# Kernel tuning notes

Measured on AMD Instinct MI355X. Metric: run time of the kernel, lower is better.

Reference implementation:

```python
import jax, jax.numpy as jnp
import numpy as np

N1, N2, D, F = 8192, 8192, 1024, 800


def setup_inputs() -> dict:
    key = jax.random.key(0)
    ks = jax.random.split(key, 10)
    s = 1.0 / np.sqrt(D)
    return {
        "m1": jax.random.normal(ks[0], (N1, D), jnp.float32),
        "m2": jax.random.normal(ks[1], (N2, D), jnp.float32),
        "Wf1": jax.random.normal(ks[2], (F, D), jnp.float32) * s,
        "bf1": jax.random.normal(ks[3], (F,), jnp.float32) * 0.01,
        "Wf2": jax.random.normal(ks[4], (F, D), jnp.float32) * s,
        "bf2": jax.random.normal(ks[5], (F,), jnp.float32) * 0.01,
        "W1": jax.random.normal(ks[6], (F, D), jnp.float32) * s,
        "b1": jax.random.normal(ks[7], (F,), jnp.float32) * 0.01,
        "W2": jax.random.normal(ks[8], (F, D), jnp.float32) * s,
        "b2": jax.random.normal(ks[9], (F,), jnp.float32) * 0.01,
    }


def reference(m1, m2, Wf1, bf1, Wf2, bf2, W1, b1, W2, b2):
    # raw_prod: [N1, N2]
    raw = jnp.einsum('id,jd->ij', m1, m2)
    alpha2 = jax.nn.softmax(raw, axis=-1)        # rows over m2: [N1, N2]
    alpha1 = jax.nn.softmax(raw.T, axis=-1)      # rows over m1: [N2, N1]
    attended_m1 = alpha1 @ m1                    # [N2, D]
    attended_m2 = alpha2 @ m2                    # [N1, D]
    # eval mode: dropout is identity
    filter1 = jax.nn.sigmoid((attended_m2 @ Wf1.T + bf1).mean(0))  # [F]
    filter2 = jax.nn.sigmoid((attended_m1 @ Wf2.T + bf2).mean(0))  # [F]
    transformed_m1 = jnp.tanh(attended_m1 @ W1.T + b1).mean(0)     # [F]
    transformed_m2 = jnp.tanh(attended_m2 @ W2.T + b2).mean(0)     # [F]
    return (transformed_m1 * filter1, transformed_m2 * filter2)
```

## Files before the change

### kernel.cpp

```cpp
#include <hip/hip_runtime.h>

typedef __attribute__((ext_vector_type(8))) short s8v;
typedef __attribute__((ext_vector_type(4))) float f4v;
typedef __attribute__((ext_vector_type(4))) unsigned short us4v;
typedef __attribute__((ext_vector_type(8))) unsigned short us8v;
typedef _Float16 h8v __attribute__((ext_vector_type(8)));

#define MFMA(a, b, c) __builtin_amdgcn_mfma_f32_16x16x32_bf16(a, b, c, 0, 0, 0)
#define GLOAD16(g, l)                                                          \
  __builtin_amdgcn_global_load_lds((const __attribute__((address_space(1))) void*)(g), \
                                   (__attribute__((address_space(3))) void*)(l), 16, 0, 0)

#define L2E 1.44269504088896f
#define C128L2E 184.6649652337873f

__device__ __forceinline__ unsigned short f2bf(float x) {
  unsigned int u = __float_as_uint(x);
  u += 0x7fffu + ((u >> 16) & 1u);
  return (unsigned short)(u >> 16);
}
__device__ __forceinline__ float bf2f(unsigned short h) {
  return __uint_as_float(((unsigned int)h) << 16);
}
__device__ __forceinline__ float f16bits2f(unsigned short u) {
  union { unsigned short us; _Float16 f; } cv; cv.us = u; return (float)cv.f;
}

__global__ void k_zero(float* p, int n) {
  int i = blockIdx.x * 256 + threadIdx.x;
  if (i < n) p[i] = 0.f;
}

__global__ __launch_bounds__(256) void k_wbf(const float* __restrict__ W,
                                             unsigned short* __restrict__ wb) {
  int idx = blockIdx.x * 256 + threadIdx.x;
  int f = idx >> 10;
  wb[idx] = f2bf((f < 800) ? W[idx] : 0.f);
}

__global__ __launch_bounds__(256) void k_prep(const float* __restrict__ in,
                                              unsigned short* __restrict__ outb,
                                              unsigned short* __restrict__ outT) {
  __shared__ float lf[64 * 68];
  int bx = blockIdx.x;
  int rb = bx >> 4, cb = bx & 15;
  long r0 = (long)rb * 64, c0 = (long)cb * 64;
  int tid = threadIdx.x;
#pragma unroll
  for (int q = 0; q < 4; ++q) {
    int fid = tid + 256 * q;
    int r = fid >> 4, c4 = fid & 15;
    f4v v = *(const f4v*)&in[(r0 + r) * 1024 + c0 + 4 * c4];
    *(f4v*)&lf[r * 68 + 4 * c4] = v;
    us4v h;
#pragma unroll
    for (int e = 0; e < 4; ++e) h[e] = f2bf(v[e]);
    *(us4v*)&outb[(r0 + r) * 1024 + c0 + 4 * c4] = h;
  }
  __syncthreads();
#pragma unroll
  for (int q = 0; q < 4; ++q) {
    int fid = tid + 256 * q;
    int oc = fid >> 4, or4 = fid & 15;
    us4v h;
#pragma unroll
    for (int e = 0; e < 4; ++e) h[e] = f2bf(lf[(4 * or4 + e) * 68 + oc]);
    *(us4v*)&outT[(c0 + oc) * 8192 + r0 + 4 * or4] = h;
  }
}

__global__ __launch_bounds__(512, 2) void k_gemm_raw8(const unsigned short* __restrict__ m1b,
                                                      const unsigned short* __restrict__ m2b,
                                                      _Float16* __restrict__ rawh,
                                                      float* __restrict__ row_s,
                                                      float* __restrict__ col_s) {
  __shared__ unsigned short LDS[65536];
  const int tid = threadIdx.x, lane = tid & 63, wid = tid >> 6;
  const int wr = wid >> 2, wc = wid & 3;
  const int x = lane >> 4;

  int swz = ((int)blockIdx.x & 7) * 128 + ((int)blockIdx.x >> 3);
  const long i0 = (long)(swz >> 5) * 256;
  const long j0 = (long)(swz & 31) * 256;

  const unsigned short* gA[2];
  const unsigned short* gB[2];
  int ldst[2];
#pragma unroll
  for (int s = 0; s < 2; ++s) {
    int c = s * 512 + tid;
    int r = c >> 2, qp = c & 3;
    int ql = qp ^ ((r >> 1) & 3);
    gA[s] = m1b + (i0 + r) * 1024 + ql * 8;
    gB[s] = m2b + (j0 + r) * 1024 + ql * 8;
    ldst[s] = c * 8;
  }
  int offA[8], offB[4];
#pragma unroll
  for (int m = 0; m < 8; ++m) {
    int rr = wr * 128 + m * 16 + (lane & 15);
    offA[m] = (rr * 4 + (x ^ ((rr >> 1) & 3))) * 8;
  }
#pragma unroll
  for (int n = 0; n < 4; ++n) {
    int cc = wc * 64 + n * 16 + (lane & 15);
    offB[n] = (cc * 4 + (x ^ ((cc >> 1) & 3))) * 8;
  }

  f4v acc[8][4];
#pragma unroll
  for (int m = 0; m < 8; ++m)
#pragma unroll
    for (int n = 0; n < 4; ++n) acc[m][n] = (f4v)0.f;

#define STG(u, kt)                                                            \
  do {                                                                        \
    _Pragma("unroll") for (int s = 0; s < 2; ++s)                             \
        GLOAD16(gA[s] + (kt) * 32, &LDS[(u) * 16384 + ldst[s]]);              \
    _Pragma("unroll") for (int s = 0; s < 2; ++s)                             \
        GLOAD16(gB[s] + (kt) * 32, &LDS[(u) * 16384 + 8192 + ldst[s]]);       \
  } while (0)

  STG(0, 0); STG(1, 1); STG(2, 2);

  for (int kt = 0; kt < 32; ++kt) {
    const int u = kt & 3;
    if (kt < 30)      asm volatile("s_waitcnt vmcnt(8)" ::: "memory");
    else if (kt == 30) asm volatile("s_waitcnt vmcnt(4)" ::: "memory");
    else               asm volatile("s_waitcnt vmcnt(0)" ::: "memory");
    asm volatile("s_barrier" ::: "memory");
    __builtin_amdgcn_sched_barrier(0);
    const int Ab = u * 16384, Bb = u * 16384 + 8192;
    s8v af[8], bf[4];
#pragma unroll
    for (int m = 0; m < 8; ++m) af[m] = *(const s8v*)&LDS[Ab + offA[m]];
#pragma unroll
    for (int n = 0; n < 4; ++n) bf[n] = *(const s8v*)&LDS[Bb + offB[n]];
    if (kt < 29) STG((kt + 3) & 3, kt + 3);
    asm volatile("s_waitcnt lgkmcnt(0)" ::: "memory");
    __builtin_amdgcn_sched_barrier(0);
    __builtin_amdgcn_s_setprio(1);
#pragma unroll
    for (int m = 0; m < 8; ++m)
#pragma unroll
      for (int n = 0; n < 4; ++n)
        acc[m][n] = MFMA(af[m], bf[n], acc[m][n]);
    __builtin_amdgcn_s_setprio(0);
  }
#undef STG

  float* rsf = (float*)LDS;
  float* csf = rsf + 256;
  if (tid < 256) { rsf[tid] = 0.f; csf[tid] = 0.f; }
  __syncthreads();
  float cls[4] = {0.f, 0.f, 0.f, 0.f};
#pragma unroll
  for (int m = 0; m < 8; ++m) {
    long rbase = i0 + wr * 128 + m * 16 + x * 4;
#pragma unroll
    for (int r = 0; r < 4; ++r) {
      float rsum = 0.f;
#pragma unroll
      for (int n = 0; n < 4; ++n) {
        long col = j0 + wc * 64 + n * 16 + (lane & 15);
        _Float16 hv = (_Float16)acc[m][n][r];
        rawh[(rbase + r) * 8192 + col] = hv;
        float e = exp2f(fmaf((float)hv, L2E, -C128L2E));
        rsum += e;
        cls[n] += e;
      }
      rsum += __shfl_xor(rsum, 1);
      rsum += __shfl_xor(rsum, 2);
      rsum += __shfl_xor(rsum, 4);
      rsum += __shfl_xor(rsum, 8);
      if ((lane & 15) == 0)
        atomicAdd(&rsf[wr * 128 + m * 16 + x * 4 + r], rsum);
    }
  }
#pragma unroll
  for (int n = 0; n < 4; ++n) {
    cls[n] += __shfl_xor(cls[n], 16);
    cls[n] += __shfl_xor(cls[n], 32);
    if (lane < 16) atomicAdd(&csf[wc * 64 + n * 16 + lane], cls[n]);
  }
  __syncthreads();
  if (tid < 256) {
    atomicAdd(&row_s[i0 + tid], rsf[tid]);
    atomicAdd(&col_s[j0 + tid], csf[tid]);
  }
}

__global__ __launch_bounds__(256) void k_fin(const float* __restrict__ s,
                                             float* __restrict__ o) {
  int i = blockIdx.x * 256 + threadIdx.x;
  o[i] = C128L2E + log2f(s[i]);
}

__global__ __launch_bounds__(512, 2) void k_gemm_att8(const unsigned short* __restrict__ P,
                                                      const unsigned short* __restrict__ BT,
                                                      unsigned short* __restrict__ attb,
                                                      float* __restrict__ meanv) {
  __shared__ unsigned short LDS[49152];
  const int tid = threadIdx.x, lane = tid & 63, wid = tid >> 6;
  const int wr = wid >> 1, wc = wid & 1;
  const int x = lane >> 4;

  int swz = ((int)blockIdx.x & 7) * 32 + ((int)blockIdx.x >> 3);
  const long i0 = (long)(swz >> 3) * 256;
  const long d0 = (long)(swz & 7) * 128;

  const unsigned short* gA[2];
  const unsigned short* gB0;
  int ldstA[2], ldstB0;
#pragma unroll
  for (int s = 0; s < 2; ++s) {
    int c = s * 512 + tid;
    int r = c >> 2, qp = c & 3;
    int ql = qp ^ ((r >> 1) & 3);
    gA[s] = P + (i0 + r) * 8192 + ql * 8;
    ldstA[s] = c * 8;
  }
  {
    int c = tid;
    int r = c >> 2, qp = c & 3;
    int ql = qp ^ ((r >> 1) & 3);
    gB0 = BT + (d0 + r) * 8192 + ql * 8;
    ldstB0 = c * 8;
  }
  int offA[4], offB[4];
#pragma unroll
  for (int m = 0; m < 4; ++m) {
    int rr = wr * 64 + m * 16 + (lane & 15);
    offA[m] = (rr * 4 + (x ^ ((rr >> 1) & 3))) * 8;
  }
#pragma unroll
  for (int n = 0; n < 4; ++n) {
    int cc = wc * 64 + n * 16 + (lane & 15);
    offB[n] = (cc * 4 + (x ^ ((cc >> 1) & 3))) * 8;
  }

  f4v acc[4][4];
#pragma unroll
  for (int m = 0; m < 4; ++m)
#pragma unroll
    for (int n = 0; n < 4; ++n) acc[m][n] = (f4v)0.f;

#define STGA(u, kt)                                                           \
  do {                                                                        \
    _Pragma("unroll") for (int s = 0; s < 2; ++s)                             \
        GLOAD16(gA[s] + (kt) * 32, &LDS[(u) * 12288 + ldstA[s]]);             \
    GLOAD16(gB0 + (kt) * 32, &LDS[(u) * 12288 + 8192 + ldstB0]);              \
  } while (0)

  STGA(0, 0); STGA(1, 1); STGA(2, 2);

  for (int kt = 0; kt < 256; ++kt) {
    const int u = kt & 3;
    if (kt < 254)       asm volatile("s_waitcnt vmcnt(6)" ::: "memory");
    else if (kt == 254) asm volatile("s_waitcnt vmcnt(3)" ::: "memory");
    else                asm volatile("s_waitcnt vmcnt(0)" ::: "memory");
    asm volatile("s_barrier" ::: "memory");
    __builtin_amdgcn_sched_barrier(0);
    const int Ab = u * 12288, Bb = u * 12288 + 8192;
    s8v af[4], bf[4];
#pragma unroll
    for (int m = 0; m < 4; ++m) af[m] = *(const s8v*)&LDS[Ab + offA[m]];
#pragma unroll
    for (int n = 0; n < 4; ++n) bf[n] = *(const s8v*)&LDS[Bb + offB[n]];
    if (kt < 253) STGA((kt + 3) & 3, kt + 3);
    asm volatile("s_waitcnt lgkmcnt(0)" ::: "memory");
    __builtin_amdgcn_sched_barrier(0);
    __builtin_amdgcn_s_setprio(1);
#pragma unroll
    for (int m = 0; m < 4; ++m)
#pragma unroll
      for (int n = 0; n < 4; ++n)
        acc[m][n] = MFMA(af[m], bf[n], acc[m][n]);
    __builtin_amdgcn_s_setprio(0);
  }
#undef STGA

#pragma unroll
  for (int n = 0; n < 4; ++n) {
    long colg = d0 + wc * 64 + n * 16 + (lane & 15);
    float s = 0.f;
#pragma unroll
    for (int m = 0; m < 4; ++m) {
      long rowg = i0 + wr * 64 + m * 16 + x * 4;
      f4v a = acc[m][n];
#pragma unroll
      for (int r = 0; r < 4; ++r) {
        attb[(rowg + r) * 1024 + colg] = f2bf(a[r]);
        s += a[r];
      }
    }
    s += __shfl_xor(s, 16);
    s += __shfl_xor(s, 32);
    if (lane < 16) atomicAdd(&meanv[d0 + wc * 64 + n * 16 + lane], s);
  }
}

__global__ __launch_bounds__(256) void k_texp_ip(unsigned short* buf,
                                                 const float* __restrict__ hh) {
  __shared__ unsigned short lt[2][64 * 80];
  int a = blockIdx.x >> 7, b = blockIdx.x & 127;
  if (a > b) return;
  const int tid = threadIdx.x;
  const int r = tid & 63;
  const int cw = tid >> 6;
  const int ntile = (a == b) ? 1 : 2;

  for (int t = 0; t < ntile; ++t) {
    long ro = (long)(t == 0 ? a : b) * 64;
    long co = (long)(t == 0 ? b : a) * 64;
#pragma unroll
    for (int q = 0; q < 2; ++q) {
      int c8 = cw + 4 * q;
      us8v u = *(const us8v*)&buf[(ro + r) * 8192 + co + c8 * 8];
      f4v hA = *(const f4v*)&hh[co + c8 * 8];
      f4v hB = *(const f4v*)&hh[co + c8 * 8 + 4];
#pragma unroll
      for (int e = 0; e < 8; ++e) {
        float hv = (e < 4) ? hA[e] : hB[e - 4];
        lt[t][(c8 * 8 + e) * 80 + r] = f2bf(exp2f(fmaf(f16bits2f(u[e]), L2E, -hv)));
      }
    }
  }
  __syncthreads();
  for (int t = 0; t < ntile; ++t) {
    long dr = (long)(t == 0 ? b : a) * 64;
    long dc = (long)(t == 0 ? a : b) * 64;
#pragma unroll
    for (int q = 0; q < 2; ++q) {
      int fid = tid + 256 * q;
      int jr = fid >> 3, c8 = fid & 7;
      us8v o = *(const us8v*)&lt[t][jr * 80 + c8 * 8];
      *(us8v*)&buf[(dr + jr) * 8192 + dc + c8 * 8] = o;
    }
  }
}

__global__ __launch_bounds__(256) void k_prow_ip(unsigned short* buf,
                                                 const float* __restrict__ hh,
                                                 const float* __restrict__ rm2) {
  __shared__ unsigned short lt[2][64 * 80];
  int a = blockIdx.x >> 7, b = blockIdx.x & 127;
  if (a > b) return;
  const int tid = threadIdx.x;
  const int r = tid & 63;
  const int cw = tid >> 6;
  const int ntile = (a == b) ? 1 : 2;

  for (int t = 0; t < ntile; ++t) {
    long ro = (long)(t == 0 ? a : b) * 64;
    long co = (long)(t == 0 ? b : a) * 64;
    float hj;
#pragma unroll
    for (int q = 0; q < 2; ++q) {
      int c8 = cw + 4 * q;
      us8v u = *(const us8v*)&buf[(ro + r) * 8192 + co + c8 * 8];
      if (q == 0) hj = hh[ro + r];
      f4v rA = *(const f4v*)&rm2[co + c8 * 8];
      f4v rB = *(const f4v*)&rm2[co + c8 * 8 + 4];
#pragma unroll
      for (int e = 0; e < 8; ++e) {
        float rv = (e < 4) ? rA[e] : rB[e - 4];
        float sc = exp2f(fminf(hj - rv, 120.f));
        lt[t][(c8 * 8 + e) * 80 + r] = f2bf(bf2f(u[e]) * sc);
      }
    }
  }
  __syncthreads();
  for (int t = 0; t < ntile; ++t) {
    long dr = (long)(t == 0 ? b : a) * 64;
    long dc = (long)(t == 0 ? a : b) * 64;
#pragma unroll
    for (int q = 0; q < 2; ++q) {
      int fid = tid + 256 * q;
      int ir = fid >> 3, c8 = fid & 7;
      us8v o = *(const us8v*)&lt[t][ir * 80 + c8 * 8];
      *(us8v*)&buf[(dr + ir) * 8192 + dc + c8 * 8] = o;
    }
  }
}

__global__ __launch_bounds__(256) void k_gemm_tanh(const unsigned short* __restrict__ attb,
                                                   const unsigned short* __restrict__ Wb,
                                                   const float* __restrict__ bias,
                                                   float* __restrict__ acct) {
  __shared__ unsigned short As[128 * 32], Bs[128 * 32];
  const int tid = threadIdx.x, lane = tid & 63, wv = tid >> 6;
  const int wrow = wv >> 1, wcol = wv & 1;
  int sw = ((int)blockIdx.x & 7) * 56 + ((int)blockIdx.x >> 3);
  const long i0 = (long)(sw / 7) * 128;
  const long f0 = (long)(sw % 7) * 128;

  const int r16 = lane >> 2;
  const int sslot = (lane & 3) ^ ((r16 >> 1) & 3);
  const unsigned short* gA0 = &attb[(i0 + 32 * wv + r16) * 1024 + sslot * 8];
  const unsigned short* gA1 = gA0 + 16 * 1024;
  const unsigned short* gB0 = &Wb[(f0 + 32 * wv + r16) * 1024 + sslot * 8];
  const unsigned short* gB1 = gB0 + 16 * 1024;
  unsigned short* lA0 = &As[(32 * wv) * 32];
  unsigned short* lA1 = &As[(32 * wv + 16) * 32];
  unsigned short* lB0 = &Bs[(32 * wv) * 32];
  unsigned short* lB1 = &Bs[(32 * wv + 16) * 32];

  f4v acc[4][4];
#pragma unroll
  for (int a = 0; a < 4; ++a)
#pragma unroll
    for (int b = 0; b < 4; ++b) acc[a][b] = (f4v)0.f;

  for (int kt = 0; kt < 32; ++kt) {
    GLOAD16(gA0 + kt * 32, lA0);
    GLOAD16(gA1 + kt * 32, lA1);
    GLOAD16(gB0 + kt * 32, lB0);
    GLOAD16(gB1 + kt * 32, lB1);
    __syncthreads();
    const int kkx = lane >> 4;
    s8v af[4], bf[4];
#pragma unroll
    for (int mf = 0; mf < 4; ++mf) {
      int rr = wrow * 64 + mf * 16 + (lane & 15);
      af[mf] = *(const s8v*)&As[rr * 32 + (kkx ^ ((rr >> 1) & 3)) * 8];
      int cc = wcol * 64 + mf * 16 + (lane & 15);
      bf[mf] = *(const s8v*)&Bs[cc * 32 + (kkx ^ ((cc >> 1) & 3)) * 8];
    }
#pragma unroll
    for (int mf = 0; mf < 4; ++mf)
#pragma unroll
      for (int nf = 0; nf < 4; ++nf)
        acc[mf][nf] = MFMA(af[mf], bf[nf], acc[mf][nf]);
    __syncthreads();
  }
#pragma unroll
  for (int nf = 0; nf < 4; ++nf) {
    long colg = f0 + wcol * 64 + nf * 16 + (lane & 15);
    float bv = (colg < 800) ? bias[colg] : 0.f;
    float s = 0.f;
#pragma unroll
    for (int mf = 0; mf < 4; ++mf) {
      f4v a = acc[mf][nf];
#pragma unroll
      for (int r = 0; r < 4; ++r) s += tanhf(a[r] + bv);
    }
    s += __shfl_xor(s, 16);
    s += __shfl_xor(s, 32);
    if (lane < 16) atomicAdd(&acct[f0 + wcol * 64 + nf * 16 + lane], s);
  }
}

__global__ __launch_bounds__(256) void k_filt(const float* __restrict__ Wf1,
                                              const float* __restrict__ bf1,
                                              const float* __restrict__ Wf2,
                                              const float* __restrict__ bf2,
                                              const float* __restrict__ mean2,
                                              const float* __restrict__ mean1,
                                              float* __restrict__ filt1,
                                              float* __restrict__ filt2) {
  int wv = threadIdx.x >> 6, lane = threadIdx.x & 63;
  int gid = blockIdx.x * 4 + wv;
  const float* Wr;
  const float* mv;
  float b;
  float* outp;
  if (gid < 800) {
    Wr = Wf1 + (long)gid * 1024; mv = mean2; b = bf1[gid]; outp = filt1 + gid;
  } else {
    int f = gid - 800;
    Wr = Wf2 + (long)f * 1024; mv = mean1; b = bf2[f]; outp = filt2 + f;
  }
  float s = 0.f;
#pragma unroll
  for (int q = 0; q < 16; ++q) s += mv[lane + 64 * q] * Wr[lane + 64 * q];
#pragma unroll
  for (int off = 32; off >= 1; off >>= 1) s += __shfl_xor(s, off);
  if (lane == 0) *outp = 1.f / (1.f + __expf(-(s * (1.f / 8192.f) + b)));
}

__global__ void k_final(const float* __restrict__ acct1, const float* __restrict__ acct2,
                        const float* __restrict__ filt1, const float* __restrict__ filt2,
                        float* __restrict__ out) {
  int i = blockIdx.x * 256 + threadIdx.x;
  if (i < 800) {
    out[i] = acct1[i] * (1.f / 8192.f) * filt1[i];
    out[800 + i] = acct2[i] * (1.f / 8192.f) * filt2[i];
  }
}

extern "C" void kernel_launch(void* const* d_in, const int* in_sizes, int n_in,
                              void* d_out, int out_size, void* d_ws, size_t ws_size,
                              hipStream_t stream) {
  (void)in_sizes; (void)n_in; (void)out_size;
  const float* m1  = (const float*)d_in[0];
  const float* m2  = (const float*)d_in[1];
  const float* Wf1 = (const float*)d_in[2];
  const float* bf1 = (const float*)d_in[3];
  const float* Wf2 = (const float*)d_in[4];
  const float* bf2 = (const float*)d_in[5];
  const float* W1  = (const float*)d_in[6];
  const float* b1  = (const float*)d_in[7];
  const float* W2  = (const float*)d_in[8];
  const float* b2  = (const float*)d_in[9];
  float* out = (float*)d_out;
  char* ws = (char*)d_ws;

  _Float16* rawh       = (_Float16*)(ws);
  unsigned short* rawu = (unsigned short*)(ws);
  unsigned short* m1T  = (unsigned short*)(ws + 134217728UL);
  unsigned short* m2T  = (unsigned short*)(ws + 150994944UL);
  unsigned short* m1b  = (unsigned short*)(ws + 167772160UL);
  unsigned short* m2b  = (unsigned short*)(ws + 184549376UL);
  unsigned short* att1 = (unsigned short*)(ws + 167772160UL);
  unsigned short* att2 = (unsigned short*)(ws + 184549376UL);
  unsigned short* W1b  = (unsigned short*)(ws + 201326592UL);
  unsigned short* W2b  = (unsigned short*)(ws + 203161600UL);
  float* rm2   = (float*)(ws + 204996608UL);
  float* hh    = (float*)(ws + 205029376UL);
  float* row_s = (float*)(ws + 205062144UL);
  float* col_s = (float*)(ws + 205094912UL);
  float* mean1 = (float*)(ws + 205127680UL);
  float* mean2 = (float*)(ws + 205131776UL);
  float* acct1 = (float*)(ws + 205135872UL);
  float* acct2 = (float*)(ws + 205139968UL);
  float* filt1 = (float*)(ws + 205144064UL);
  float* filt2 = (float*)(ws + 205148160UL);

  if (ws_size < 207246592UL) return;

  k_zero<<<80, 256, 0, stream>>>(row_s, 20480);
  k_wbf<<<3584, 256, 0, stream>>>(W1, W1b);
  k_wbf<<<3584, 256, 0, stream>>>(W2, W2b);
  k_prep<<<2048, 256, 0, stream>>>(m1, m1b, m1T);
  k_prep<<<2048, 256, 0, stream>>>(m2, m2b, m2T);
  k_gemm_raw8<<<1024, 512, 0, stream>>>(m1b, m2b, rawh, row_s, col_s);
  k_fin<<<64, 256, 0, stream>>>(row_s, rm2);
  k_texp_ip<<<16384, 256, 0, stream>>>(rawu, hh);
  k_gemm_att8<<<256, 512, 0, stream>>>(rawu, m1T, att1, mean1);
  k_prow_ip<<<16384, 256, 0, stream>>>(rawu, hh, rm2);
  k_gemm_att8<<<256, 512, 0, stream>>>(rawu, m2T, att2, mean2);
  k_gemm_tanh<<<448, 256, 0, stream>>>(att1, W1b, b1, acct1);
  k_gemm_tanh<<<448, 256, 0, stream>>>(att2, W2b, b2, acct2);
  k_filt<<<400, 256, 0, stream>>>(Wf1, bf1, Wf2, bf2, mean2, mean1, filt1, filt2);
  k_final<<<4, 256, 0, stream>>>(acct1, acct2, filt1, filt2, out);
}
```

Baseline: 605.9 us.

## Store exp-shifted probabilities once and defer softmax normalization into attention GEMMs

The raw GEMM epilogue now writes bf16 exp(raw-128) directly instead of fp16 raw logits. Both attention GEMMs consume this same unnormalized P, and divide each output row by its row or column sum in the epilogue. This removes the log-sum kernel, the exponentiation inside the transpose pass, and the whole rescaling pass over the 8192x8192 matrix, leaving only a plain in-place transpose. The cost is that both softmax directions now share one fixed shift, so probabilities are stored unnormalized in bf16, which depends on the logit range staying within float range.

```diff
diff --git a/kernel.cpp b/kernel.cpp
--- a/kernel.cpp
+++ b/kernel.cpp
@@ -4,7 +4,6 @@
 typedef __attribute__((ext_vector_type(4))) float f4v;
 typedef __attribute__((ext_vector_type(4))) unsigned short us4v;
 typedef __attribute__((ext_vector_type(8))) unsigned short us8v;
-typedef _Float16 h8v __attribute__((ext_vector_type(8)));
 
 #define MFMA(a, b, c) __builtin_amdgcn_mfma_f32_16x16x32_bf16(a, b, c, 0, 0, 0)
 #define GLOAD16(g, l)                                                          \
@@ -21,9 +20,6 @@
 }
 __device__ __forceinline__ float bf2f(unsigned short h) {
   return __uint_as_float(((unsigned int)h) << 16);
-}
-__device__ __forceinline__ float f16bits2f(unsigned short u) {
-  union { unsigned short us; _Float16 f; } cv; cv.us = u; return (float)cv.f;
 }
 
 __global__ void k_zero(float* p, int n) {
@@ -71,7 +67,7 @@
 
 __global__ __launch_bounds__(512, 2) void k_gemm_raw8(const unsigned short* __restrict__ m1b,
                                                       const unsigned short* __restrict__ m2b,
-                                                      _Float16* __restrict__ rawh,
+                                                      unsigned short* __restrict__ Pb,
                                                       float* __restrict__ row_s,
                                                       float* __restrict__ col_s) {
   __shared__ unsigned short LDS[65536];
@@ -163,9 +159,8 @@
 #pragma unroll
       for (int n = 0; n < 4; ++n) {
         long col = j0 + wc * 64 + n * 16 + (lane & 15);
-        _Float16 hv = (_Float16)acc[m][n][r];
-        rawh[(rbase + r) * 8192 + col] = hv;
-        float e = exp2f(fmaf((float)hv, L2E, -C128L2E));
+        float e = exp2f(fmaf(acc[m][n][r], L2E, -C128L2E));
+        Pb[(rbase + r) * 8192 + col] = f2bf(e);
         rsum += e;
         cls[n] += e;
       }
@@ -190,16 +185,11 @@
   }
 }
 
-__global__ __launch_bounds__(256) void k_fin(const float* __restrict__ s,
-                                             float* __restrict__ o) {
-  int i = blockIdx.x * 256 + threadIdx.x;
-  o[i] = C128L2E + log2f(s[i]);
-}
-
 __global__ __launch_bounds__(512, 2) void k_gemm_att8(const unsigned short* __restrict__ P,
                                                       const unsigned short* __restrict__ BT,
                                                       unsigned short* __restrict__ attb,
-                                                      float* __restrict__ meanv) {
+                                                      float* __restrict__ meanv,
+                                                      const float* __restrict__ divv) {
   __shared__ unsigned short LDS[49152];
   const int tid = threadIdx.x, lane = tid & 63, wid = tid >> 6;
   const int wr = wid >> 1, wc = wid & 1;
@@ -280,6 +270,13 @@
   }
 #undef STGA
 
+  float inv[4][4];
+#pragma unroll
+  for (int m = 0; m < 4; ++m)
+#pragma unroll
+    for (int r = 0; r < 4; ++r)
+      inv[m][r] = 1.f / divv[i0 + wr * 64 + m * 16 + x * 4 + r];
+
 #pragma unroll
   for (int n = 0; n < 4; ++n) {
     long colg = d0 + wc * 64 + n * 16 + (lane & 15);
@@ -290,8 +287,9 @@
       f4v a = acc[m][n];
 #pragma unroll
       for (int r = 0; r < 4; ++r) {
-        attb[(rowg + r) * 1024 + colg] = f2bf(a[r]);
-        s += a[r];
+        float val = a[r] * inv[m][r];
+        attb[(rowg + r) * 1024 + colg] = f2bf(val);
+        s += val;
       }
     }
     s += __shfl_xor(s, 16);
@@ -300,8 +298,7 @@
   }
 }
 
-__global__ __launch_bounds__(256) void k_texp_ip(unsigned short* buf,
-                                                 const float* __restrict__ hh) {
+__global__ __launch_bounds__(256) void k_tr(unsigned short* buf) {
   __shared__ unsigned short lt[2][64 * 80];
   int a = blockIdx.x >> 7, b = blockIdx.x & 127;
   if (a > b) return;
@@ -317,13 +314,8 @@
     for (int q = 0; q < 2; ++q) {
       int c8 = cw + 4 * q;
       us8v u = *(const us8v*)&buf[(ro + r) * 8192 + co + c8 * 8];
-      f4v hA = *(const f4v*)&hh[co + c8 * 8];
-      f4v hB = *(const f4v*)&hh[co + c8 * 8 + 4];
-#pragma unroll
-      for (int e = 0; e < 8; ++e) {
-        float hv = (e < 4) ? hA[e] : hB[e - 4];
-        lt[t][(c8 * 8 + e) * 80 + r] = f2bf(exp2f(fmaf(f16bits2f(u[e]), L2E, -hv)));
-      }
+#pragma unroll
+      for (int e = 0; e < 8; ++e) lt[t][(c8 * 8 + e) * 80 + r] = u[e];
     }
   }
   __syncthreads();
@@ -336,50 +328,6 @@
       int jr = fid >> 3, c8 = fid & 7;
       us8v o = *(const us8v*)&lt[t][jr * 80 + c8 * 8];
       *(us8v*)&buf[(dr + jr) * 8192 + dc + c8 * 8] = o;
-    }
-  }
-}
-
-__global__ __launch_bounds__(256) void k_prow_ip(unsigned short* buf,
-                                                 const float* __restrict__ hh,
-                                                 const float* __restrict__ rm2) {
-  __shared__ unsigned short lt[2][64 * 80];
-  int a = blockIdx.x >> 7, b = blockIdx.x & 127;
-  if (a > b) return;
-  const int tid = threadIdx.x;
-  const int r = tid & 63;
-  const int cw = tid >> 6;
-  const int ntile = (a == b) ? 1 : 2;
-
-  for (int t = 0; t < ntile; ++t) {
-    long ro = (long)(t == 0 ? a : b) * 64;
-    long co = (long)(t == 0 ? b : a) * 64;
-    float hj;
-#pragma unroll
-    for (int q = 0; q < 2; ++q) {
-      int c8 = cw + 4 * q;
-      us8v u = *(const us8v*)&buf[(ro + r) * 8192 + co + c8 * 8];
-      if (q == 0) hj = hh[ro + r];
-      f4v rA = *(const f4v*)&rm2[co + c8 * 8];
-      f4v rB = *(const f4v*)&rm2[co + c8 * 8 + 4];
-#pragma unroll
-      for (int e = 0; e < 8; ++e) {
-        float rv = (e < 4) ? rA[e] : rB[e - 4];
-        float sc = exp2f(fminf(hj - rv, 120.f));
-        lt[t][(c8 * 8 + e) * 80 + r] = f2bf(bf2f(u[e]) * sc);
-      }
-    }
-  }
-  __syncthreads();
-  for (int t = 0; t < ntile; ++t) {
-    long dr = (long)(t == 0 ? b : a) * 64;
-    long dc = (long)(t == 0 ? a : b) * 64;
-#pragma unroll
-    for (int q = 0; q < 2; ++q) {
-      int fid = tid + 256 * q;
-      int ir = fid >> 3, c8 = fid & 7;
-      us8v o = *(const us8v*)&lt[t][ir * 80 + c8 * 8];
-      *(us8v*)&buf[(dr + ir) * 8192 + dc + c8 * 8] = o;
     }
   }
 }
@@ -506,8 +454,7 @@
   float* out = (float*)d_out;
   char* ws = (char*)d_ws;
 
-  _Float16* rawh       = (_Float16*)(ws);
-  unsigned short* rawu = (unsigned short*)(ws);
+  unsigned short* Pb   = (unsigned short*)(ws);
   unsigned short* m1T  = (unsigned short*)(ws + 134217728UL);
   unsigned short* m2T  = (unsigned short*)(ws + 150994944UL);
   unsigned short* m1b  = (unsigned short*)(ws + 167772160UL);
@@ -516,8 +463,6 @@
   unsigned short* att2 = (unsigned short*)(ws + 184549376UL);
   unsigned short* W1b  = (unsigned short*)(ws + 201326592UL);
   unsigned short* W2b  = (unsigned short*)(ws + 203161600UL);
-  float* rm2   = (float*)(ws + 204996608UL);
-  float* hh    = (float*)(ws + 205029376UL);
   float* row_s = (float*)(ws + 205062144UL);
   float* col_s = (float*)(ws + 205094912UL);
   float* mean1 = (float*)(ws + 205127680UL);
@@ -534,12 +479,10 @@
   k_wbf<<<3584, 256, 0, stream>>>(W2, W2b);
   k_prep<<<2048, 256, 0, stream>>>(m1, m1b, m1T);
   k_prep<<<2048, 256, 0, stream>>>(m2, m2b, m2T);
-  k_gemm_raw8<<<1024, 512, 0, stream>>>(m1b, m2b, rawh, row_s, col_s);
-  k_fin<<<64, 256, 0, stream>>>(row_s, rm2);
-  k_texp_ip<<<16384, 256, 0, stream>>>(rawu, hh);
-  k_gemm_att8<<<256, 512, 0, stream>>>(rawu, m1T, att1, mean1);
-  k_prow_ip<<<16384, 256, 0, stream>>>(rawu, hh, rm2);
-  k_gemm_att8<<<256, 512, 0, stream>>>(rawu, m2T, att2, mean2);
+  k_gemm_raw8<<<1024, 512, 0, stream>>>(m1b, m2b, Pb, row_s, col_s);
+  k_gemm_att8<<<256, 512, 0, stream>>>(Pb, m2T, att2, mean2, row_s);
+  k_tr<<<16384, 256, 0, stream>>>(Pb);
+  k_gemm_att8<<<256, 512, 0, stream>>>(Pb, m1T, att1, mean1, col_s);
   k_gemm_tanh<<<448, 256, 0, stream>>>(att1, W1b, b1, acct1);
   k_gemm_tanh<<<448, 256, 0, stream>>>(att2, W2b, b2, acct2);
   k_filt<<<400, 256, 0, stream>>>(Wf1, bf1, Wf2, bf2, mean2, mean1, filt1, filt2);
```

Result: faster. 543.3 us, median of 3 (-10.3%).
